# Optimization experiments

Hardware: AMD Instinct MI355X
Metric: run time of the kernel (lower is better)

## Reference

```python
import jax, jax.numpy as jnp
import numpy as np

EPS = 1e-7
FEAT_DIM = 128
N_DATA = 100000
NCE_K = 16384
NCE_T = 0.07


def _l2norm(x):
    # Normalize(power=2): x / (sum(x^2, axis=1)^(1/2))
    return x / jnp.sqrt(jnp.sum(x * x, axis=1, keepdims=True))


def _embed(x, W, b):
    return _l2norm(x @ W.T + b)


def _contrast_loss(x, n_data):
    # x: [B, K+1] of (unnormalized) probabilities; col 0 = positive
    bsz = x.shape[0]
    m = x.shape[1] - 1
    Pn = 1.0 / float(n_data)
    c = m * Pn + EPS
    log_D1 = jnp.log(x[:, 0] / (x[:, 0] + c))          # positives
    log_D0 = jnp.log((m * Pn) / (x[:, 1:] + c))         # negatives
    return -(log_D1.sum() + log_D0.sum()) / bsz


def setup_inputs() -> dict:
    key = jax.random.key(0)
    ks = jax.random.split(key, 10)
    s_dim, t_dim = 1024, 2048
    B = 64
    stdv = 1.0 / np.sqrt(FEAT_DIM / 3.0)
    inp = {
        "f_s": jax.random.normal(ks[0], (B, s_dim), dtype=jnp.float32),
        "f_t": jax.random.normal(ks[1], (B, t_dim), dtype=jnp.float32),
        "idx": jax.random.randint(ks[2], (B,), 0, N_DATA),
        "contrast_idx": jax.random.randint(ks[3], (B, NCE_K + 1), 0, N_DATA),
        # Embed params (linear): Linear(dim_in, feat_dim)
        "Ws": jax.random.normal(ks[4], (FEAT_DIM, s_dim), dtype=jnp.float32) / np.sqrt(s_dim),
        "bs": jnp.zeros((FEAT_DIM,), dtype=jnp.float32),
        "Wt": jax.random.normal(ks[5], (FEAT_DIM, t_dim), dtype=jnp.float32) / np.sqrt(t_dim),
        "bt": jnp.zeros((FEAT_DIM,), dtype=jnp.float32),
        # memory banks, init uniform(-stdv, stdv) as in CRD ContrastMemory
        "memory_v1": jax.random.uniform(ks[6], (N_DATA, FEAT_DIM), jnp.float32, -stdv, stdv),
        "memory_v2": jax.random.uniform(ks[7], (N_DATA, FEAT_DIM), jnp.float32, -stdv, stdv),
    }
    return inp


def reference(f_s, f_t, idx, contrast_idx, Ws, bs, Wt, bt, memory_v1, memory_v2):
    v_s = _embed(f_s, Ws, bs)   # [B, D]
    v_t = _embed(f_t, Wt, bt)   # [B, D]

    # idx.select(1,0).copy_(y): column 0 is the positive index
    idx_all = jnp.concatenate([idx[:, None], contrast_idx[:, 1:]], axis=1)  # [B, K+1]

    # gather from memory banks + bmm similarity
    w1 = memory_v1[idx_all]   # [B, K+1, D] (v_t side bank)
    w2 = memory_v2[idx_all]   # [B, K+1, D] (v_s side bank)
    out_t = jnp.exp(jnp.einsum('bkd,bd->bk', w1, v_t) / NCE_T)  # out_v2
    out_s = jnp.exp(jnp.einsum('bkd,bd->bk', w2, v_s) / NCE_T)  # out_v1

    # Z set on first batch: Z = out.mean() * n_data (detached constant)
    Z_s = jax.lax.stop_gradient(out_s.mean()) * N_DATA
    Z_t = jax.lax.stop_gradient(out_t.mean()) * N_DATA
    out_s = out_s / Z_s
    out_t = out_t / Z_t

    s_loss = _contrast_loss(out_s, N_DATA)
    t_loss = _contrast_loss(out_t, N_DATA)
    return s_loss + t_loss
```

## Files before the change

kernel.cpp:

```cpp
#include <hip/hip_runtime.h>

#define NDATA 100000
#define KP1 16385
#define BSZ 64
#define PTOT (BSZ * KP1)
#define NTILES 1563
#define INV_T (1.0f / 0.07f)

typedef short short8 __attribute__((ext_vector_type(8)));
typedef float f32x4 __attribute__((ext_vector_type(4)));

__device__ __forceinline__ float wave_reduce64(float v) {
    #pragma unroll
    for (int off = 32; off >= 1; off >>= 1) v += __shfl_xor(v, off);
    return v;
}

__device__ __forceinline__ unsigned short f2bf(float f) {
    unsigned u = __float_as_uint(f);
    u += 0x7FFFu + ((u >> 16) & 1u);
    return (unsigned short)(u >> 16);
}

__device__ __forceinline__ float dot4(float4 a, float4 b, float acc) {
    acc = fmaf(a.x, b.x, acc);
    acc = fmaf(a.y, b.y, acc);
    acc = fmaf(a.z, b.z, acc);
    return fmaf(a.w, b.w, acc);
}

__global__ __launch_bounds__(256) void embed_kernel(
    const float* __restrict__ fs, const float* __restrict__ ft,
    const float* __restrict__ Ws, const float* __restrict__ bs,
    const float* __restrict__ Wt, const float* __restrict__ bt,
    float* __restrict__ vraw_s, float* __restrict__ vraw_t,
    float* __restrict__ n2s, float* __restrict__ n2t)
{
    __shared__ __align__(16) float4 FS[512];
    __shared__ __align__(16) float4 FT[1024];

    const int t  = threadIdx.x;
    const int dt = blockIdx.x;
    const int b0 = blockIdx.y * 2;

    for (int q = t; q < 512; q += 256) {
        const int b = q >> 8, i = q & 255;
        FS[q] = ((const float4*)(fs + (size_t)(b0 + b) * 1024))[i];
    }
    for (int q = t; q < 1024; q += 256) {
        const int b = q >> 9, i = q & 511;
        FT[q] = ((const float4*)(ft + (size_t)(b0 + b) * 2048))[i];
    }
    __syncthreads();

    const int w = t >> 6, lane = t & 63;
    float ps0 = 0.0f, ps1 = 0.0f, pt0 = 0.0f, pt1 = 0.0f;

    #pragma unroll
    for (int r = 0; r < 4; ++r) {
        const int d = dt * 16 + w * 4 + r;
        const float4* wrow = (const float4*)(Ws + (size_t)d * 1024);
        float a0 = 0.0f, a1 = 0.0f;
        #pragma unroll
        for (int i = 0; i < 4; ++i) {
            const float4 wv = wrow[i * 64 + lane];
            a0 = dot4(wv, FS[i * 64 + lane], a0);
            a1 = dot4(wv, FS[256 + i * 64 + lane], a1);
        }
        a0 = wave_reduce64(a0) + bs[d];
        a1 = wave_reduce64(a1) + bs[d];
        ps0 = fmaf(a0, a0, ps0);
        ps1 = fmaf(a1, a1, ps1);
        if (lane == 0) {
            vraw_s[(size_t)b0 * 128 + d]       = a0;
            vraw_s[(size_t)(b0 + 1) * 128 + d] = a1;
        }
    }
    #pragma unroll
    for (int r = 0; r < 4; ++r) {
        const int d = dt * 16 + w * 4 + r;
        const float4* wrow = (const float4*)(Wt + (size_t)d * 2048);
        float a0 = 0.0f, a1 = 0.0f;
        #pragma unroll
        for (int i = 0; i < 8; ++i) {
            const float4 wv = wrow[i * 64 + lane];
            a0 = dot4(wv, FT[i * 64 + lane], a0);
            a1 = dot4(wv, FT[512 + i * 64 + lane], a1);
        }
        a0 = wave_reduce64(a0) + bt[d];
        a1 = wave_reduce64(a1) + bt[d];
        pt0 = fmaf(a0, a0, pt0);
        pt1 = fmaf(a1, a1, pt1);
        if (lane == 0) {
            vraw_t[(size_t)b0 * 128 + d]       = a0;
            vraw_t[(size_t)(b0 + 1) * 128 + d] = a1;
        }
    }
    if (lane == 0) {
        atomicAdd(&n2s[b0],     ps0);
        atomicAdd(&n2s[b0 + 1], ps1);
        atomicAdd(&n2t[b0],     pt0);
        atomicAdd(&n2t[b0 + 1], pt1);
    }
}

__device__ __forceinline__ void stage_tile(
    unsigned short* __restrict__ dst, const float* __restrict__ src,
    int row0, int t, bool clampRows)
{
    #pragma unroll
    for (int i = 0; i < 8; ++i) {
        const int q = t + i * 256;
        const int r = q >> 5, c = q & 31;
        int gr = row0 + r;
        if (clampRows && gr >= NDATA) gr = NDATA - 1;
        const float4 v = ((const float4*)(src + (size_t)gr * 128))[c];
        ushort4 u;
        u.x = f2bf(v.x); u.y = f2bf(v.y); u.z = f2bf(v.z); u.w = f2bf(v.w);
        *(ushort4*)&dst[r * 128 + (((c >> 1) ^ (r & 15)) * 8) + (c & 1) * 4] = u;
    }
}

__global__ __launch_bounds__(256) void sgemm_kernel(
    const float* __restrict__ m1, const float* __restrict__ m2,
    const float* __restrict__ vraw_s, const float* __restrict__ vraw_t,
    float* __restrict__ S1, float* __restrict__ S2)
{
    __shared__ __align__(16) unsigned short Vs[64 * 128];
    __shared__ __align__(16) unsigned short As[2][64 * 128];

    const int t = threadIdx.x;
    const int bank = blockIdx.y;
    const float* __restrict__ bankp = bank ? m2 : m1;
    const float* __restrict__ vp    = bank ? vraw_s : vraw_t;
    float* __restrict__ Sp          = bank ? S2 : S1;

    const int tile0  = blockIdx.x * 4;
    const int ntiles = min(4, NTILES - tile0);

    stage_tile(Vs, vp, 0, t, false);
    stage_tile(As[0], bankp, tile0 * 64, t, true);
    __syncthreads();

    const int lane = t & 63;
    const int m  = lane & 15;
    const int q4 = lane >> 4;
    const int m0 = (t >> 6) * 16;

    for (int it = 0; it < ntiles; ++it) {
        if (it + 1 < ntiles)
            stage_tile(As[(it + 1) & 1], bankp, (tile0 + it + 1) * 64, t, true);

        const unsigned short* A = As[it & 1];
        const int row0 = (tile0 + it) * 64;

        short8 af[4];
        #pragma unroll
        for (int kk = 0; kk < 4; ++kk)
            af[kk] = *(const short8*)&A[(m0 + m) * 128 + (((kk * 4 + q4) ^ m) * 8)];

        const int rbase = row0 + m0 + q4 * 4;
        const bool valid = (rbase < NDATA);

        #pragma unroll
        for (int n0 = 0; n0 < 64; n0 += 16) {
            f32x4 acc = {0.f, 0.f, 0.f, 0.f};
            #pragma unroll
            for (int kk = 0; kk < 4; ++kk) {
                short8 bf = *(const short8*)&Vs[(n0 + m) * 128 + (((kk * 4 + q4) ^ m) * 8)];
                acc = __builtin_amdgcn_mfma_f32_16x16x32_bf16(af[kk], bf, acc, 0, 0, 0);
            }
            if (valid)
                *(f32x4*)(Sp + (size_t)(n0 + m) * NDATA + rbase) = acc;
        }
        __syncthreads();
    }
}

__global__ __launch_bounds__(256) void gather_kernel(
    const int* __restrict__ cidx,
    const float* __restrict__ S1, const float* __restrict__ S2,
    const float* __restrict__ n2t, const float* __restrict__ n2s,
    float* __restrict__ acc)
{
    const int b = blockIdx.x, part = blockIdx.y, t = threadIdx.x;
    const float sct = INV_T * rsqrtf(n2t[b]);
    const float scs = INV_T * rsqrtf(n2s[b]);
    const float* __restrict__ S1b = S1 + (size_t)b * NDATA;
    const float* __restrict__ S2b = S2 + (size_t)b * NDATA;
    const int kbase = part * 2048 + 1;

    int rows[8];
    #pragma unroll
    for (int j = 0; j < 8; ++j)
        rows[j] = cidx[(size_t)b * KP1 + kbase + j * 256 + t];

    float v1[8], v2[8];
    #pragma unroll
    for (int j = 0; j < 8; ++j) {
        v1[j] = S1b[rows[j]];
        v2[j] = S2b[rows[j]];
    }

    float seT = 0.f, se2T = 0.f, seS = 0.f, se2S = 0.f;
    #pragma unroll
    for (int j = 0; j < 8; ++j) {
        const float e1 = __expf(v1[j] * sct);
        const float e2 = __expf(v2[j] * scs);
        seT += e1; se2T = fmaf(e1, e1, se2T);
        seS += e2; se2S = fmaf(e2, e2, se2S);
    }

    seT = wave_reduce64(seT);  se2T = wave_reduce64(se2T);
    seS = wave_reduce64(seS);  se2S = wave_reduce64(se2S);

    __shared__ float red[4][4];
    if ((t & 63) == 0) {
        const int w = t >> 6;
        red[w][0] = seT; red[w][1] = se2T; red[w][2] = seS; red[w][3] = se2S;
    }
    __syncthreads();
    if (t < 4)
        atomicAdd(&acc[t], red[0][t] + red[1][t] + red[2][t] + red[3][t]);
}

__global__ __launch_bounds__(64) void final_kernel(
    const int* __restrict__ idx,
    const float* __restrict__ S1, const float* __restrict__ S2,
    const float* __restrict__ n2t, const float* __restrict__ n2s,
    const float* __restrict__ acc, float* __restrict__ out)
{
    const int b = threadIdx.x;
    const float c = 0.16384f + 1e-7f;
    const int row = idx[b];

    const float e1p = __expf(S1[(size_t)b * NDATA + row] * INV_T * rsqrtf(n2t[b]));
    const float e2p = __expf(S2[(size_t)b * NDATA + row] * INV_T * rsqrtf(n2s[b]));

    const float pseT = wave_reduce64(e1p);
    const float pseS = wave_reduce64(e2p);

    const float seT_neg = acc[0], se2T_neg = acc[1];
    const float seS_neg = acc[2], se2S_neg = acc[3];

    const float zn = (float)PTOT / (float)NDATA;
    const float invZt = zn / (seT_neg + pseT);
    const float invZs = zn / (seS_neg + pseS);

    const float PB = (float)(PTOT - BSZ);
    const float LOG_MPN_C = -6.1035156e-7f;
    const float ic = 1.0f / c;

    const float negT = PB * LOG_MPN_C
                     - seT_neg * invZt * ic
                     + 0.5f * se2T_neg * invZt * invZt * ic * ic;
    const float negS = PB * LOG_MPN_C
                     - seS_neg * invZs * ic
                     + 0.5f * se2S_neg * invZs * invZs * ic * ic;

    const float x0t = e1p * invZt, x0s = e2p * invZs;
    float pos = __logf(x0t / (x0t + c)) + __logf(x0s / (x0s + c));
    pos = wave_reduce64(pos);

    if (b == 0) out[0] = -(negT + negS + pos) * (1.0f / 64.0f);
}

extern "C" void kernel_launch(void* const* d_in, const int* in_sizes, int n_in,
                              void* d_out, int out_size, void* d_ws, size_t ws_size,
                              hipStream_t stream) {
    const float* fs   = (const float*)d_in[0];
    const float* ft   = (const float*)d_in[1];
    const int*   idx  = (const int*)d_in[2];
    const int*   cidx = (const int*)d_in[3];
    const float* Ws   = (const float*)d_in[4];
    const float* bs   = (const float*)d_in[5];
    const float* Wt   = (const float*)d_in[6];
    const float* bt   = (const float*)d_in[7];
    const float* m1   = (const float*)d_in[8];
    const float* m2   = (const float*)d_in[9];
    float* out = (float*)d_out;

    float* ws     = (float*)d_ws;
    float* n2t    = ws;
    float* n2s    = ws + 64;
    float* acc    = ws + 128;
    float* vraw_s = ws + 144;
    float* vraw_t = vraw_s + 8192;
    float* S1     = vraw_t + 8192;
    float* S2     = S1 + (size_t)BSZ * NDATA;

    hipMemsetAsync(ws, 0, 144 * sizeof(float), stream);

    embed_kernel<<<dim3(8, 32), dim3(256), 0, stream>>>(
        fs, ft, Ws, bs, Wt, bt, vraw_s, vraw_t, n2s, n2t);
    sgemm_kernel<<<dim3(391, 2), dim3(256), 0, stream>>>(
        m1, m2, vraw_s, vraw_t, S1, S2);
    gather_kernel<<<dim3(64, 8), dim3(256), 0, stream>>>(
        cidx, S1, S2, n2t, n2s, acc);
    final_kernel<<<dim3(1), dim3(64), 0, stream>>>(
        idx, S1, S2, n2t, n2s, acc, out);
}
```

Measured before the change: 199.5 us.

## Store similarity matrix in bf16, drop LDS staging, fuse final into gather

The dense similarity GEMM now loads memory-bank rows directly into registers as MFMA fragments, with a grid-stride loop over 16-row chunks and no LDS double buffer. Results are written as bf16, which halves the write traffic and the later gather reads. The memset and the separate final kernel are removed: norm partials are reduced in the GEMM kernel, and the last gather block computes the loss through an atomic counter. This lowers launch count and memory traffic but adds bf16 rounding on the logits before exp.

```diff
diff --git a/kernel.cpp b/kernel.cpp
--- a/kernel.cpp
+++ b/kernel.cpp
@@ -4,8 +4,9 @@
 #define KP1 16385
 #define BSZ 64
 #define PTOT (BSZ * KP1)
-#define NTILES 1563
+#define NCHUNK 6250
 #define INV_T (1.0f / 0.07f)
+#define GX 320
 
 typedef short short8 __attribute__((ext_vector_type(8)));
 typedef float f32x4 __attribute__((ext_vector_type(4)));
@@ -20,6 +21,10 @@
     unsigned u = __float_as_uint(f);
     u += 0x7FFFu + ((u >> 16) & 1u);
     return (unsigned short)(u >> 16);
+}
+
+__device__ __forceinline__ float bf2f(unsigned short u) {
+    return __uint_as_float((unsigned)u << 16);
 }
 
 __device__ __forceinline__ float dot4(float4 a, float4 b, float acc) {
@@ -29,15 +34,25 @@
     return fmaf(a.w, b.w, acc);
 }
 
+__device__ __forceinline__ short8 pack_bf8(float4 x0, float4 x1) {
+    short8 s;
+    s[0] = (short)f2bf(x0.x); s[1] = (short)f2bf(x0.y);
+    s[2] = (short)f2bf(x0.z); s[3] = (short)f2bf(x0.w);
+    s[4] = (short)f2bf(x1.x); s[5] = (short)f2bf(x1.y);
+    s[6] = (short)f2bf(x1.z); s[7] = (short)f2bf(x1.w);
+    return s;
+}
+
 __global__ __launch_bounds__(256) void embed_kernel(
     const float* __restrict__ fs, const float* __restrict__ ft,
     const float* __restrict__ Ws, const float* __restrict__ bs,
     const float* __restrict__ Wt, const float* __restrict__ bt,
     float* __restrict__ vraw_s, float* __restrict__ vraw_t,
-    float* __restrict__ n2s, float* __restrict__ n2t)
+    float* __restrict__ n2part_s, float* __restrict__ n2part_t)
 {
     __shared__ __align__(16) float4 FS[512];
     __shared__ __align__(16) float4 FT[1024];
+    __shared__ float rS[4][2], rT[4][2];
 
     const int t  = threadIdx.x;
     const int dt = blockIdx.x;
@@ -97,97 +112,98 @@
         }
     }
     if (lane == 0) {
-        atomicAdd(&n2s[b0],     ps0);
-        atomicAdd(&n2s[b0 + 1], ps1);
-        atomicAdd(&n2t[b0],     pt0);
-        atomicAdd(&n2t[b0 + 1], pt1);
-    }
-}
-
-__device__ __forceinline__ void stage_tile(
-    unsigned short* __restrict__ dst, const float* __restrict__ src,
-    int row0, int t, bool clampRows)
-{
-    #pragma unroll
-    for (int i = 0; i < 8; ++i) {
-        const int q = t + i * 256;
-        const int r = q >> 5, c = q & 31;
-        int gr = row0 + r;
-        if (clampRows && gr >= NDATA) gr = NDATA - 1;
-        const float4 v = ((const float4*)(src + (size_t)gr * 128))[c];
-        ushort4 u;
-        u.x = f2bf(v.x); u.y = f2bf(v.y); u.z = f2bf(v.z); u.w = f2bf(v.w);
-        *(ushort4*)&dst[r * 128 + (((c >> 1) ^ (r & 15)) * 8) + (c & 1) * 4] = u;
+        rS[w][0] = ps0; rS[w][1] = ps1;
+        rT[w][0] = pt0; rT[w][1] = pt1;
+    }
+    __syncthreads();
+    if (t == 0) {
+        n2part_s[dt * 64 + b0]     = rS[0][0] + rS[1][0] + rS[2][0] + rS[3][0];
+        n2part_s[dt * 64 + b0 + 1] = rS[0][1] + rS[1][1] + rS[2][1] + rS[3][1];
+        n2part_t[dt * 64 + b0]     = rT[0][0] + rT[1][0] + rT[2][0] + rT[3][0];
+        n2part_t[dt * 64 + b0 + 1] = rT[0][1] + rT[1][1] + rT[2][1] + rT[3][1];
     }
 }
 
 __global__ __launch_bounds__(256) void sgemm_kernel(
     const float* __restrict__ m1, const float* __restrict__ m2,
     const float* __restrict__ vraw_s, const float* __restrict__ vraw_t,
-    float* __restrict__ S1, float* __restrict__ S2)
+    const float* __restrict__ n2part_s, const float* __restrict__ n2part_t,
+    float* __restrict__ n2s, float* __restrict__ n2t,
+    float* __restrict__ acc, int* __restrict__ counter,
+    unsigned short* __restrict__ S1, unsigned short* __restrict__ S2)
 {
-    __shared__ __align__(16) unsigned short Vs[64 * 128];
-    __shared__ __align__(16) unsigned short As[2][64 * 128];
-
-    const int t = threadIdx.x;
     const int bank = blockIdx.y;
     const float* __restrict__ bankp = bank ? m2 : m1;
     const float* __restrict__ vp    = bank ? vraw_s : vraw_t;
-    float* __restrict__ Sp          = bank ? S2 : S1;
-
-    const int tile0  = blockIdx.x * 4;
-    const int ntiles = min(4, NTILES - tile0);
-
-    stage_tile(Vs, vp, 0, t, false);
-    stage_tile(As[0], bankp, tile0 * 64, t, true);
-    __syncthreads();
-
-    const int lane = t & 63;
+    unsigned short* __restrict__ Sp = bank ? S2 : S1;
+
+    if (blockIdx.x == 0) {
+        if (threadIdx.x < 64) {
+            const int b = threadIdx.x;
+            const float* np = bank ? n2part_s : n2part_t;
+            float s = 0.0f;
+            #pragma unroll
+            for (int p = 0; p < 8; ++p) s += np[p * 64 + b];
+            (bank ? n2s : n2t)[b] = s;
+            if (b < 2) acc[bank * 2 + b] = 0.0f;
+        } else if (threadIdx.x == 64 && bank == 0) {
+            counter[0] = 0;
+        }
+    }
+
+    const int lane = threadIdx.x & 63;
     const int m  = lane & 15;
     const int q4 = lane >> 4;
-    const int m0 = (t >> 6) * 16;
-
-    for (int it = 0; it < ntiles; ++it) {
-        if (it + 1 < ntiles)
-            stage_tile(As[(it + 1) & 1], bankp, (tile0 + it + 1) * 64, t, true);
-
-        const unsigned short* A = As[it & 1];
-        const int row0 = (tile0 + it) * 64;
-
+
+    short8 vf[4][4];
+    #pragma unroll
+    for (int n0i = 0; n0i < 4; ++n0i) {
+        const float* vb = vp + (size_t)(n0i * 16 + m) * 128 + q4 * 8;
+        #pragma unroll
+        for (int kk = 0; kk < 4; ++kk)
+            vf[n0i][kk] = pack_bf8(*(const float4*)(vb + kk * 32),
+                                   *(const float4*)(vb + kk * 32 + 4));
+    }
+
+    const int w0 = blockIdx.x * 4 + (threadIdx.x >> 6);
+    for (int c = w0; c < NCHUNK; c += GX * 4) {
+        const float* ap = bankp + ((size_t)c * 16 + m) * 128 + q4 * 8;
+        float4 a0[4], a1[4];
+        #pragma unroll
+        for (int kk = 0; kk < 4; ++kk) {
+            a0[kk] = *(const float4*)(ap + kk * 32);
+            a1[kk] = *(const float4*)(ap + kk * 32 + 4);
+        }
         short8 af[4];
         #pragma unroll
-        for (int kk = 0; kk < 4; ++kk)
-            af[kk] = *(const short8*)&A[(m0 + m) * 128 + (((kk * 4 + q4) ^ m) * 8)];
-
-        const int rbase = row0 + m0 + q4 * 4;
-        const bool valid = (rbase < NDATA);
-
-        #pragma unroll
-        for (int n0 = 0; n0 < 64; n0 += 16) {
-            f32x4 acc = {0.f, 0.f, 0.f, 0.f};
+        for (int kk = 0; kk < 4; ++kk) af[kk] = pack_bf8(a0[kk], a1[kk]);
+
+        #pragma unroll
+        for (int n0i = 0; n0i < 4; ++n0i) {
+            f32x4 a4 = {0.f, 0.f, 0.f, 0.f};
             #pragma unroll
-            for (int kk = 0; kk < 4; ++kk) {
-                short8 bf = *(const short8*)&Vs[(n0 + m) * 128 + (((kk * 4 + q4) ^ m) * 8)];
-                acc = __builtin_amdgcn_mfma_f32_16x16x32_bf16(af[kk], bf, acc, 0, 0, 0);
-            }
-            if (valid)
-                *(f32x4*)(Sp + (size_t)(n0 + m) * NDATA + rbase) = acc;
-        }
-        __syncthreads();
+            for (int kk = 0; kk < 4; ++kk)
+                a4 = __builtin_amdgcn_mfma_f32_16x16x32_bf16(af[kk], vf[n0i][kk], a4, 0, 0, 0);
+            uint2 pk;
+            pk.x = (unsigned)f2bf(a4[0]) | ((unsigned)f2bf(a4[1]) << 16);
+            pk.y = (unsigned)f2bf(a4[2]) | ((unsigned)f2bf(a4[3]) << 16);
+            *(uint2*)(Sp + (size_t)(n0i * 16 + m) * NDATA + c * 16 + q4 * 4) = pk;
+        }
     }
 }
 
 __global__ __launch_bounds__(256) void gather_kernel(
-    const int* __restrict__ cidx,
-    const float* __restrict__ S1, const float* __restrict__ S2,
+    const int* __restrict__ idx, const int* __restrict__ cidx,
+    const unsigned short* __restrict__ S1, const unsigned short* __restrict__ S2,
     const float* __restrict__ n2t, const float* __restrict__ n2s,
-    float* __restrict__ acc)
+    float* __restrict__ acc, int* __restrict__ counter,
+    float* __restrict__ out)
 {
     const int b = blockIdx.x, part = blockIdx.y, t = threadIdx.x;
     const float sct = INV_T * rsqrtf(n2t[b]);
     const float scs = INV_T * rsqrtf(n2s[b]);
-    const float* __restrict__ S1b = S1 + (size_t)b * NDATA;
-    const float* __restrict__ S2b = S2 + (size_t)b * NDATA;
+    const unsigned short* __restrict__ S1b = S1 + (size_t)b * NDATA;
+    const unsigned short* __restrict__ S2b = S2 + (size_t)b * NDATA;
     const int kbase = part * 2048 + 1;
 
     int rows[8];
@@ -198,8 +214,8 @@
     float v1[8], v2[8];
     #pragma unroll
     for (int j = 0; j < 8; ++j) {
-        v1[j] = S1b[rows[j]];
-        v2[j] = S2b[rows[j]];
+        v1[j] = bf2f(S1b[rows[j]]);
+        v2[j] = bf2f(S2b[rows[j]]);
     }
 
     float seT = 0.f, se2T = 0.f, seS = 0.f, se2S = 0.f;
@@ -215,41 +231,44 @@
     seS = wave_reduce64(seS);  se2S = wave_reduce64(se2S);
 
     __shared__ float red[4][4];
+    __shared__ int lastFlag;
     if ((t & 63) == 0) {
         const int w = t >> 6;
         red[w][0] = seT; red[w][1] = se2T; red[w][2] = seS; red[w][3] = se2S;
     }
     __syncthreads();
-    if (t < 4)
+    if (t < 4) {
         atomicAdd(&acc[t], red[0][t] + red[1][t] + red[2][t] + red[3][t]);
-}
-
-__global__ __launch_bounds__(64) void final_kernel(
-    const int* __restrict__ idx,
-    const float* __restrict__ S1, const float* __restrict__ S2,
-    const float* __restrict__ n2t, const float* __restrict__ n2s,
-    const float* __restrict__ acc, float* __restrict__ out)
-{
-    const int b = threadIdx.x;
-    const float c = 0.16384f + 1e-7f;
-    const int row = idx[b];
-
-    const float e1p = __expf(S1[(size_t)b * NDATA + row] * INV_T * rsqrtf(n2t[b]));
-    const float e2p = __expf(S2[(size_t)b * NDATA + row] * INV_T * rsqrtf(n2s[b]));
-
+        __threadfence();
+    }
+    __syncthreads();
+    if (t == 0) lastFlag = (atomicAdd(counter, 1) == 64 * 8 - 1);
+    __syncthreads();
+    if (!lastFlag) return;
+
+    __shared__ float av[4];
+    if (t < 4) av[t] = atomicAdd(&acc[t], 0.0f);
+    __syncthreads();
+    if (t >= 64) return;
+
+    const int bb = t;
+    const int row = idx[bb];
+    const float e1p = __expf(bf2f(S1[(size_t)bb * NDATA + row]) * INV_T * rsqrtf(n2t[bb]));
+    const float e2p = __expf(bf2f(S2[(size_t)bb * NDATA + row]) * INV_T * rsqrtf(n2s[bb]));
     const float pseT = wave_reduce64(e1p);
     const float pseS = wave_reduce64(e2p);
 
-    const float seT_neg = acc[0], se2T_neg = acc[1];
-    const float seS_neg = acc[2], se2S_neg = acc[3];
+    const float seT_neg = av[0], se2T_neg = av[1];
+    const float seS_neg = av[2], se2S_neg = av[3];
 
     const float zn = (float)PTOT / (float)NDATA;
     const float invZt = zn / (seT_neg + pseT);
     const float invZs = zn / (seS_neg + pseS);
 
+    const float c  = 0.16384f + 1e-7f;
+    const float ic = 1.0f / c;
     const float PB = (float)(PTOT - BSZ);
     const float LOG_MPN_C = -6.1035156e-7f;
-    const float ic = 1.0f / c;
 
     const float negT = PB * LOG_MPN_C
                      - seT_neg * invZt * ic
@@ -262,7 +281,7 @@
     float pos = __logf(x0t / (x0t + c)) + __logf(x0s / (x0s + c));
     pos = wave_reduce64(pos);
 
-    if (b == 0) out[0] = -(negT + negS + pos) * (1.0f / 64.0f);
+    if (bb == 0) out[0] = -(negT + negS + pos) * (1.0f / 64.0f);
 }
 
 extern "C" void kernel_launch(void* const* d_in, const int* in_sizes, int n_in,
@@ -280,23 +299,23 @@
     const float* m2   = (const float*)d_in[9];
     float* out = (float*)d_out;
 
-    float* ws     = (float*)d_ws;
-    float* n2t    = ws;
-    float* n2s    = ws + 64;
-    float* acc    = ws + 128;
-    float* vraw_s = ws + 144;
-    float* vraw_t = vraw_s + 8192;
-    float* S1     = vraw_t + 8192;
-    float* S2     = S1 + (size_t)BSZ * NDATA;
-
-    hipMemsetAsync(ws, 0, 144 * sizeof(float), stream);
+    float* ws       = (float*)d_ws;
+    float* n2t      = ws;
+    float* n2s      = ws + 64;
+    float* acc      = ws + 128;
+    int*   counter  = (int*)(ws + 132);
+    float* n2part_s = ws + 136;
+    float* n2part_t = ws + 648;
+    float* vraw_s   = ws + 1160;
+    float* vraw_t   = vraw_s + 8192;
+    unsigned short* S1 = (unsigned short*)(vraw_t + 8192);
+    unsigned short* S2 = S1 + (size_t)BSZ * NDATA;
 
     embed_kernel<<<dim3(8, 32), dim3(256), 0, stream>>>(
-        fs, ft, Ws, bs, Wt, bt, vraw_s, vraw_t, n2s, n2t);
-    sgemm_kernel<<<dim3(391, 2), dim3(256), 0, stream>>>(
-        m1, m2, vraw_s, vraw_t, S1, S2);
+        fs, ft, Ws, bs, Wt, bt, vraw_s, vraw_t, n2part_s, n2part_t);
+    sgemm_kernel<<<dim3(GX, 2), dim3(256), 0, stream>>>(
+        m1, m2, vraw_s, vraw_t, n2part_s, n2part_t,
+        n2s, n2t, acc, counter, S1, S2);
     gather_kernel<<<dim3(64, 8), dim3(256), 0, stream>>>(
-        cidx, S1, S2, n2t, n2s, acc);
-    final_kernel<<<dim3(1), dim3(64), 0, stream>>>(
-        idx, S1, S2, n2t, n2s, acc, out);
-}
+        idx, cidx, S1, S2, n2t, n2s, acc, counter, out);
+}
```

After: 202.6 us. No clear change (+1.6%).
